# Performance work log

Hardware: AMD Instinct MI355X
Metric: run time of the kernel (lower is better)

Reference implementation:

```python
import jax, jax.numpy as jnp
import numpy as np

N, D, C, O = 65536, 256, 1024, 64

def setup_inputs() -> dict:
    key = jax.random.key(0)
    k1, k2, k3, k4 = jax.random.split(key, 4)
    x = jax.random.normal(k1, (N, D), dtype=jnp.float32)
    centers = jax.random.normal(k2, (C, D), dtype=jnp.float32)
    sigma = jnp.ones((C,), dtype=jnp.float32)
    # nn.Linear(C, O): weight [O, C], bias [O]
    bound = 1.0 / np.sqrt(C)
    W = jax.random.uniform(k3, (O, C), minval=-bound, maxval=bound, dtype=jnp.float32)
    b = jax.random.uniform(k4, (O,), minval=-bound, maxval=bound, dtype=jnp.float32)
    return {"x": x, "centers": centers, "sigma": sigma, "W": W, "b": b}

def reference(x, centers, sigma, W, b):
    # dist_sq[n,c] = ||x_n - c_c||^2, via GEMM identity (same math as sum((x-c)**2))
    x_sq = jnp.sum(x * x, axis=-1, keepdims=True)              # [N,1]
    c_sq = jnp.sum(centers * centers, axis=-1)                 # [C]
    cross = jnp.einsum('nd,cd->nc', x, centers)                # [N,C]
    dist_sq = x_sq - 2.0 * cross + c_sq[None, :]               # [N,C]
    rbf = jnp.exp(-dist_sq / (2.0 * sigma ** 2 + 1e-8))        # [N,C]
    out = jnp.einsum('nc,oc->no', rbf, W) + b                  # [N,O]
    return out
```

## Files before the change

### kernel.cpp

```cpp
#include <hip/hip_runtime.h>
#include <stdint.h>

#define NROWS 65536
#define DIM   256
#define NC    1024
#define NO    64

#define BN    128
#define WROWS 32
#define BC    128
#define NTILE (NC / BC)

using bf16x8 = __bf16 __attribute__((ext_vector_type(8)));
using f32x4  = float __attribute__((ext_vector_type(4)));
using u16x4  = unsigned short __attribute__((ext_vector_type(4)));
using u32x2  = unsigned int __attribute__((ext_vector_type(2)));

#define MFMA16(a, b, c) __builtin_amdgcn_mfma_f32_16x16x32_bf16((a), (b), (c), 0, 0, 0)

__device__ inline unsigned short bf16_bits(float f) {
    __bf16 h = (__bf16)f;
    return __builtin_bit_cast(unsigned short, h);
}

__global__ __launch_bounds__(256) void prep(const float* __restrict__ cent,
                                            const float* __restrict__ sigma,
                                            const float* __restrict__ w,
                                            unsigned short* __restrict__ cbf,
                                            float* __restrict__ a2,
                                            float* __restrict__ acs,
                                            unsigned short* __restrict__ wbf) {
    const int bid = blockIdx.x;
    if (bid < 256) {
        const int wid = threadIdx.x >> 6, lane = threadIdx.x & 63;
        const int c = bid * 4 + wid;
        float4 v = ((const float4*)cent)[(size_t)c * 64 + lane];
        u16x4 o;
        o[0] = bf16_bits(v.x); o[1] = bf16_bits(v.y);
        o[2] = bf16_bits(v.z); o[3] = bf16_bits(v.w);
        const int t = c >> 7, crow = c & 127, kc = lane >> 1;
        *(u16x4*)((char*)cbf + t * 65536 + (kc * 128 + crow) * 16 + (lane & 1) * 8) = o;
        float ss = v.x * v.x + v.y * v.y + v.z * v.z + v.w * v.w;
        #pragma unroll
        for (int off = 32; off; off >>= 1) ss += __shfl_down(ss, off);
        if (lane == 0) {
            float s = sigma[c];
            float al = 1.0f / (2.0f * s * s + 1e-8f);
            a2[c] = 2.0f * al;
            acs[c] = al * ss;
        }
    } else {
        const int o = bid - 256;
        float4 v = ((const float4*)w)[(size_t)o * 256 + threadIdx.x];
        u16x4 u;
        u[0] = bf16_bits(v.x); u[1] = bf16_bits(v.y);
        u[2] = bf16_bits(v.z); u[3] = bf16_bits(v.w);
        *(u16x4*)(wbf + (size_t)o * NC + threadIdx.x * 4) = u;
    }
}

__global__ __launch_bounds__(256, 2) void rbf_main(
    const float* __restrict__ x,
    const __bf16* __restrict__ cbf, const float* __restrict__ a2,
    const float* __restrict__ acs, const __bf16* __restrict__ wbf,
    const float* __restrict__ bias, float* __restrict__ out) {

    __shared__ __bf16 cent_lds[BC * DIM];
    __shared__ __bf16 rbf_lds[4][WROWS * 64];

    const int tid  = threadIdx.x;
    const int wid  = tid >> 6;
    const int lane = tid & 63;
    const int l15  = lane & 15;
    const int hi   = lane >> 4;

    const int rowbase = blockIdx.x * BN + wid * WROWS;

    bf16x8 xf[2][8];
    float hxsq[2];
    #pragma unroll
    for (int nf = 0; nf < 2; ++nf) {
        const float* xr = x + (size_t)(rowbase + nf * 16 + l15) * DIM;
        float ss = 0.f;
        #pragma unroll
        for (int ks = 0; ks < 8; ++ks) {
            float4 a = *(const float4*)(xr + ks * 32 + hi * 8);
            float4 b = *(const float4*)(xr + ks * 32 + hi * 8 + 4);
            bf16x8 f;
            f[0] = (__bf16)a.x; f[1] = (__bf16)a.y; f[2] = (__bf16)a.z; f[3] = (__bf16)a.w;
            f[4] = (__bf16)b.x; f[5] = (__bf16)b.y; f[6] = (__bf16)b.z; f[7] = (__bf16)b.w;
            xf[nf][ks] = f;
            ss += a.x * a.x + a.y * a.y + a.z * a.z + a.w * a.w;
            ss += b.x * b.x + b.y * b.y + b.z * b.z + b.w * b.w;
        }
        ss += __shfl_xor(ss, 16);
        ss += __shfl_xor(ss, 32);
        hxsq[nf] = 0.5f * ss;
    }

    float bo[4];
    #pragma unroll
    for (int of = 0; of < 4; ++of) bo[of] = bias[of * 16 + l15];

    f32x4 oacc[2][4];
    #pragma unroll
    for (int nf = 0; nf < 2; ++nf)
        #pragma unroll
        for (int of = 0; of < 4; ++of) {
            f32x4 z = {0.f, 0.f, 0.f, 0.f};
            oacc[nf][of] = z;
        }

    #pragma unroll 1
    for (int t = 0; t < NTILE; ++t) {
        __syncthreads();
        {
            const char* src = (const char*)cbf + (size_t)t * 65536
                              + (size_t)(wid * 64 + lane) * 16;
            char* dstb = (char*)cent_lds + (wid * 64) * 16;
            #pragma unroll
            for (int i = 0; i < 16; ++i) {
                __builtin_amdgcn_global_load_lds(
                    (const __attribute__((address_space(1))) uint32_t*)(src + i * 4096),
                    (__attribute__((address_space(3))) uint32_t*)(dstb + i * 4096), 16, 0, 0);
            }
        }
        asm volatile("s_waitcnt vmcnt(0)" ::: "memory");
        __syncthreads();

        f32x4 st[8][2];
        #pragma unroll
        for (int c4 = 0; c4 < 8; ++c4)
            #pragma unroll
            for (int nf = 0; nf < 2; ++nf) {
                f32x4 z = {0.f, 0.f, 0.f, 0.f};
                st[c4][nf] = z;
            }
        #pragma unroll
        for (int ks = 0; ks < 8; ++ks) {
            bf16x8 cf[8];
            #pragma unroll
            for (int c4 = 0; c4 < 8; ++c4)
                cf[c4] = *(const bf16x8*)((const char*)cent_lds
                          + ((ks * 4 + hi) * 128 + c4 * 16 + l15) * 16);
            #pragma unroll
            for (int c4 = 0; c4 < 8; ++c4)
                #pragma unroll
                for (int nf = 0; nf < 2; ++nf)
                    st[c4][nf] = MFMA16(cf[c4], xf[nf][ks], st[c4][nf]);
        }

        char* const rbase = (char*)&rbf_lds[wid][0];
        #pragma unroll
        for (int h = 0; h < 2; ++h) {
            #pragma unroll
            for (int c4h = 0; c4h < 4; ++c4h) {
                const int c4 = h * 4 + c4h;
                const int cg = t * BC + c4 * 16 + hi * 4;
                const f32x4 a24 = *(const f32x4*)(a2 + cg);
                const f32x4 ac4 = *(const f32x4*)(acs + cg);
                #pragma unroll
                for (int nf = 0; nf < 2; ++nf) {
                    const f32x4 v = st[c4][nf];
                    float p0 = __expf(a24[0] * (v[0] - hxsq[nf]) - ac4[0]);
                    float p1 = __expf(a24[1] * (v[1] - hxsq[nf]) - ac4[1]);
                    float p2 = __expf(a24[2] * (v[2] - hxsq[nf]) - ac4[2]);
                    float p3 = __expf(a24[3] * (v[3] - hxsq[nf]) - ac4[3]);
                    u32x2 wv;
                    wv[0] = (unsigned)bf16_bits(p0) | ((unsigned)bf16_bits(p1) << 16);
                    wv[1] = (unsigned)bf16_bits(p2) | ((unsigned)bf16_bits(p3) << 16);
                    const int byte = ((c4h * 2 + (hi >> 1)) * 32 + nf * 16 + l15) * 16
                                     + (hi & 1) * 8;
                    *(u32x2*)(rbase + byte) = wv;
                }
            }
            #pragma unroll
            for (int cs = 0; cs < 2; ++cs) {
                bf16x8 pa[2];
                #pragma unroll
                for (int nf = 0; nf < 2; ++nf)
                    pa[nf] = *(const bf16x8*)(rbase
                              + ((cs * 4 + hi) * 32 + nf * 16 + l15) * 16);
                #pragma unroll
                for (int of = 0; of < 4; ++of) {
                    const bf16x8 wb = *(const bf16x8*)(wbf
                        + (size_t)(of * 16 + l15) * NC + t * BC + h * 64 + cs * 32 + hi * 8);
                    #pragma unroll
                    for (int nf = 0; nf < 2; ++nf)
                        oacc[nf][of] = MFMA16(pa[nf], wb, oacc[nf][of]);
                }
            }
        }
    }

    #pragma unroll
    for (int nf = 0; nf < 2; ++nf)
        #pragma unroll
        for (int of = 0; of < 4; ++of)
            #pragma unroll
            for (int r = 0; r < 4; ++r) {
                const int n = rowbase + nf * 16 + hi * 4 + r;
                out[(size_t)n * NO + of * 16 + l15] = oacc[nf][of][r] + bo[of];
            }
}

extern "C" void kernel_launch(void* const* d_in, const int* in_sizes, int n_in,
                              void* d_out, int out_size, void* d_ws, size_t ws_size,
                              hipStream_t stream) {
    const float* x     = (const float*)d_in[0];
    const float* cent  = (const float*)d_in[1];
    const float* sigma = (const float*)d_in[2];
    const float* W     = (const float*)d_in[3];
    const float* b     = (const float*)d_in[4];
    float* out = (float*)d_out;

    char* ws = (char*)d_ws;
    unsigned short* cbf  = (unsigned short*)(ws + 0);
    float*          a2p  = (float*)(ws + 524288);
    float*          acsp = (float*)(ws + 528384);
    unsigned short* wbf  = (unsigned short*)(ws + 532480);

    prep<<<320, 256, 0, stream>>>(cent, sigma, W, cbf, a2p, acsp, wbf);
    rbf_main<<<NROWS / BN, 256, 0, stream>>>(
        x, (const __bf16*)cbf, a2p, acsp, (const __bf16*)wbf, b, out);
}
```

Before: 169.6 us.

## Halve center tile and prefetch next tile during second GEMM

Shrinks the center tile from 128 to 64 rows, which halves the LDS footprint, and restructures the loop. The next tile's global-to-LDS load is now issued after the first GEMM and exp stage, so it overlaps the second (rbf×W) GEMM instead of stalling at the loop top. The first tile is also prefetched before the x fragments are loaded. The first GEMM is reordered per 16-center group, which cuts live accumulator registers. The cost is twice as many barriers and tile iterations.

```diff
diff --git a/kernel.cpp b/kernel.cpp
--- a/kernel.cpp
+++ b/kernel.cpp
@@ -8,7 +8,7 @@
 
 #define BN    128
 #define WROWS 32
-#define BC    128
+#define BC    64
 #define NTILE (NC / BC)
 
 using bf16x8 = __bf16 __attribute__((ext_vector_type(8)));
@@ -38,8 +38,8 @@
         u16x4 o;
         o[0] = bf16_bits(v.x); o[1] = bf16_bits(v.y);
         o[2] = bf16_bits(v.z); o[3] = bf16_bits(v.w);
-        const int t = c >> 7, crow = c & 127, kc = lane >> 1;
-        *(u16x4*)((char*)cbf + t * 65536 + (kc * 128 + crow) * 16 + (lane & 1) * 8) = o;
+        const int t = c >> 6, crow = c & 63, kc = lane >> 1;
+        *(u16x4*)((char*)cbf + t * 32768 + (kc * 64 + crow) * 16 + (lane & 1) * 8) = o;
         float ss = v.x * v.x + v.y * v.y + v.z * v.z + v.w * v.w;
         #pragma unroll
         for (int off = 32; off; off >>= 1) ss += __shfl_down(ss, off);
@@ -66,7 +66,7 @@
     const float* __restrict__ bias, float* __restrict__ out) {
 
     __shared__ __bf16 cent_lds[BC * DIM];
-    __shared__ __bf16 rbf_lds[4][WROWS * 64];
+    __shared__ __bf16 rbf_lds[4][WROWS * BC];
 
     const int tid  = threadIdx.x;
     const int wid  = tid >> 6;
@@ -75,6 +75,20 @@
     const int hi   = lane >> 4;
 
     const int rowbase = blockIdx.x * BN + wid * WROWS;
+
+    auto stage = [&](int t) {
+        const char* src = (const char*)cbf + (size_t)t * 32768
+                          + (size_t)(wid * 64 + lane) * 16;
+        char* dstb = (char*)cent_lds + (wid * 64) * 16;
+        #pragma unroll
+        for (int i = 0; i < 8; ++i) {
+            __builtin_amdgcn_global_load_lds(
+                (const __attribute__((address_space(1))) uint32_t*)(src + i * 4096),
+                (__attribute__((address_space(3))) uint32_t*)(dstb + i * 4096), 16, 0, 0);
+        }
+    };
+
+    stage(0);
 
     bf16x8 xf[2][8];
     float hxsq[2];
@@ -111,86 +125,76 @@
             oacc[nf][of] = z;
         }
 
+    asm volatile("s_waitcnt vmcnt(0)" ::: "memory");
+    __syncthreads();
+
+    char* const rbase = (char*)&rbf_lds[wid][0];
+
     #pragma unroll 1
     for (int t = 0; t < NTILE; ++t) {
+        #pragma unroll
+        for (int c4 = 0; c4 < 4; ++c4) {
+            bf16x8 cf[8];
+            #pragma unroll
+            for (int ks = 0; ks < 8; ++ks)
+                cf[ks] = *(const bf16x8*)((const char*)cent_lds
+                          + ((ks * 4 + hi) * 64 + c4 * 16 + l15) * 16);
+            f32x4 s0 = {0.f, 0.f, 0.f, 0.f};
+            f32x4 s1 = {0.f, 0.f, 0.f, 0.f};
+            #pragma unroll
+            for (int ks = 0; ks < 8; ++ks) {
+                s0 = MFMA16(cf[ks], xf[0][ks], s0);
+                s1 = MFMA16(cf[ks], xf[1][ks], s1);
+            }
+            const int cg = t * BC + c4 * 16 + hi * 4;
+            const f32x4 a24 = *(const f32x4*)(a2 + cg);
+            const f32x4 ac4 = *(const f32x4*)(acs + cg);
+            const int cc0 = (c4 * 2 + (hi >> 1)) * 32;
+            const int sub = (hi & 1) * 8;
+            {
+                float p0 = __expf(a24[0] * (s0[0] - hxsq[0]) - ac4[0]);
+                float p1 = __expf(a24[1] * (s0[1] - hxsq[0]) - ac4[1]);
+                float p2 = __expf(a24[2] * (s0[2] - hxsq[0]) - ac4[2]);
+                float p3 = __expf(a24[3] * (s0[3] - hxsq[0]) - ac4[3]);
+                u32x2 wv;
+                wv[0] = (unsigned)bf16_bits(p0) | ((unsigned)bf16_bits(p1) << 16);
+                wv[1] = (unsigned)bf16_bits(p2) | ((unsigned)bf16_bits(p3) << 16);
+                *(u32x2*)(rbase + (cc0 + l15) * 16 + sub) = wv;
+            }
+            {
+                float p0 = __expf(a24[0] * (s1[0] - hxsq[1]) - ac4[0]);
+                float p1 = __expf(a24[1] * (s1[1] - hxsq[1]) - ac4[1]);
+                float p2 = __expf(a24[2] * (s1[2] - hxsq[1]) - ac4[2]);
+                float p3 = __expf(a24[3] * (s1[3] - hxsq[1]) - ac4[3]);
+                u32x2 wv;
+                wv[0] = (unsigned)bf16_bits(p0) | ((unsigned)bf16_bits(p1) << 16);
+                wv[1] = (unsigned)bf16_bits(p2) | ((unsigned)bf16_bits(p3) << 16);
+                *(u32x2*)(rbase + (cc0 + 16 + l15) * 16 + sub) = wv;
+            }
+        }
+
         __syncthreads();
-        {
-            const char* src = (const char*)cbf + (size_t)t * 65536
-                              + (size_t)(wid * 64 + lane) * 16;
-            char* dstb = (char*)cent_lds + (wid * 64) * 16;
-            #pragma unroll
-            for (int i = 0; i < 16; ++i) {
-                __builtin_amdgcn_global_load_lds(
-                    (const __attribute__((address_space(1))) uint32_t*)(src + i * 4096),
-                    (__attribute__((address_space(3))) uint32_t*)(dstb + i * 4096), 16, 0, 0);
-            }
-        }
+        if (t + 1 < NTILE) stage(t + 1);
+
+        #pragma unroll
+        for (int cs = 0; cs < 2; ++cs) {
+            bf16x8 pa[2];
+            #pragma unroll
+            for (int nf = 0; nf < 2; ++nf)
+                pa[nf] = *(const bf16x8*)(rbase
+                          + ((cs * 4 + hi) * 32 + nf * 16 + l15) * 16);
+            #pragma unroll
+            for (int of = 0; of < 4; ++of) {
+                const bf16x8 wb = *(const bf16x8*)(wbf + (size_t)(of * 16 + l15) * NC
+                                                   + t * BC + cs * 32 + hi * 8);
+                #pragma unroll
+                for (int nf = 0; nf < 2; ++nf)
+                    oacc[nf][of] = MFMA16(pa[nf], wb, oacc[nf][of]);
+            }
+        }
+
         asm volatile("s_waitcnt vmcnt(0)" ::: "memory");
         __syncthreads();
-
-        f32x4 st[8][2];
-        #pragma unroll
-        for (int c4 = 0; c4 < 8; ++c4)
-            #pragma unroll
-            for (int nf = 0; nf < 2; ++nf) {
-                f32x4 z = {0.f, 0.f, 0.f, 0.f};
-                st[c4][nf] = z;
-            }
-        #pragma unroll
-        for (int ks = 0; ks < 8; ++ks) {
-            bf16x8 cf[8];
-            #pragma unroll
-            for (int c4 = 0; c4 < 8; ++c4)
-                cf[c4] = *(const bf16x8*)((const char*)cent_lds
-                          + ((ks * 4 + hi) * 128 + c4 * 16 + l15) * 16);
-            #pragma unroll
-            for (int c4 = 0; c4 < 8; ++c4)
-                #pragma unroll
-                for (int nf = 0; nf < 2; ++nf)
-                    st[c4][nf] = MFMA16(cf[c4], xf[nf][ks], st[c4][nf]);
-        }
-
-        char* const rbase = (char*)&rbf_lds[wid][0];
-        #pragma unroll
-        for (int h = 0; h < 2; ++h) {
-            #pragma unroll
-            for (int c4h = 0; c4h < 4; ++c4h) {
-                const int c4 = h * 4 + c4h;
-                const int cg = t * BC + c4 * 16 + hi * 4;
-                const f32x4 a24 = *(const f32x4*)(a2 + cg);
-                const f32x4 ac4 = *(const f32x4*)(acs + cg);
-                #pragma unroll
-                for (int nf = 0; nf < 2; ++nf) {
-                    const f32x4 v = st[c4][nf];
-                    float p0 = __expf(a24[0] * (v[0] - hxsq[nf]) - ac4[0]);
-                    float p1 = __expf(a24[1] * (v[1] - hxsq[nf]) - ac4[1]);
-                    float p2 = __expf(a24[2] * (v[2] - hxsq[nf]) - ac4[2]);
-                    float p3 = __expf(a24[3] * (v[3] - hxsq[nf]) - ac4[3]);
-                    u32x2 wv;
-                    wv[0] = (unsigned)bf16_bits(p0) | ((unsigned)bf16_bits(p1) << 16);
-                    wv[1] = (unsigned)bf16_bits(p2) | ((unsigned)bf16_bits(p3) << 16);
-                    const int byte = ((c4h * 2 + (hi >> 1)) * 32 + nf * 16 + l15) * 16
-                                     + (hi & 1) * 8;
-                    *(u32x2*)(rbase + byte) = wv;
-                }
-            }
-            #pragma unroll
-            for (int cs = 0; cs < 2; ++cs) {
-                bf16x8 pa[2];
-                #pragma unroll
-                for (int nf = 0; nf < 2; ++nf)
-                    pa[nf] = *(const bf16x8*)(rbase
-                              + ((cs * 4 + hi) * 32 + nf * 16 + l15) * 16);
-                #pragma unroll
-                for (int of = 0; of < 4; ++of) {
-                    const bf16x8 wb = *(const bf16x8*)(wbf
-                        + (size_t)(of * 16 + l15) * NC + t * BC + h * 64 + cs * 32 + hi * 8);
-                    #pragma unroll
-                    for (int nf = 0; nf < 2; ++nf)
-                        oacc[nf][of] = MFMA16(pa[nf], wb, oacc[nf][of]);
-                }
-            }
-        }
     }
 
     #pragma unroll
```

Result: faster. 165.5 us (-2.4%).

## Split work across wave pairs, shrink center tile, overlap next-tile staging

Applied to the files above, without the earlier changes.

The block grows to 512 threads (8 waves) arranged as 4 pairs. Each pair shares 32 rows and the two waves in a pair split the centers and output columns. The center tile shrinks to 64 so that LDS and register use per wave drop, allowing higher occupancy (launch bounds 512,4). The next center tile is loaded into LDS asynchronously while the second GEMM runs, hiding part of the global-load latency. The cost is more block-wide barriers and redundant x loads and norm computation, since both waves of a pair read the same rows.

```diff
diff --git a/kernel.cpp b/kernel.cpp
--- a/kernel.cpp
+++ b/kernel.cpp
@@ -7,8 +7,7 @@
 #define NO    64
 
 #define BN    128
-#define WROWS 32
-#define BC    128
+#define BC    64
 #define NTILE (NC / BC)
 
 using bf16x8 = __bf16 __attribute__((ext_vector_type(8)));
@@ -38,8 +37,8 @@
         u16x4 o;
         o[0] = bf16_bits(v.x); o[1] = bf16_bits(v.y);
         o[2] = bf16_bits(v.z); o[3] = bf16_bits(v.w);
-        const int t = c >> 7, crow = c & 127, kc = lane >> 1;
-        *(u16x4*)((char*)cbf + t * 65536 + (kc * 128 + crow) * 16 + (lane & 1) * 8) = o;
+        const int t = c >> 6, crow = c & 63, kc = lane >> 1;
+        *(u16x4*)((char*)cbf + t * 32768 + (kc * 64 + crow) * 16 + (lane & 1) * 8) = o;
         float ss = v.x * v.x + v.y * v.y + v.z * v.z + v.w * v.w;
         #pragma unroll
         for (int off = 32; off; off >>= 1) ss += __shfl_down(ss, off);
@@ -59,22 +58,37 @@
     }
 }
 
-__global__ __launch_bounds__(256, 2) void rbf_main(
+__global__ __launch_bounds__(512, 4) void rbf_main(
     const float* __restrict__ x,
     const __bf16* __restrict__ cbf, const float* __restrict__ a2,
     const float* __restrict__ acs, const __bf16* __restrict__ wbf,
     const float* __restrict__ bias, float* __restrict__ out) {
 
     __shared__ __bf16 cent_lds[BC * DIM];
-    __shared__ __bf16 rbf_lds[4][WROWS * 64];
+    __shared__ __bf16 rbf_lds[4][32 * BC];
 
     const int tid  = threadIdx.x;
     const int wid  = tid >> 6;
+    const int pair = wid >> 1;
+    const int half = wid & 1;
     const int lane = tid & 63;
     const int l15  = lane & 15;
     const int hi   = lane >> 4;
 
-    const int rowbase = blockIdx.x * BN + wid * WROWS;
+    const int rowbase = blockIdx.x * BN + pair * 32;
+
+    auto stage = [&](int t) {
+        const char* src = (const char*)cbf + (size_t)t * 32768 + (size_t)tid * 16;
+        char* dstb = (char*)cent_lds + (wid * 64) * 16;
+        #pragma unroll
+        for (int i = 0; i < 4; ++i) {
+            __builtin_amdgcn_global_load_lds(
+                (const __attribute__((address_space(1))) uint32_t*)(src + i * 8192),
+                (__attribute__((address_space(3))) uint32_t*)(dstb + i * 8192), 16, 0, 0);
+        }
+    };
+
+    stage(0);
 
     bf16x8 xf[2][8];
     float hxsq[2];
@@ -98,39 +112,29 @@
         hxsq[nf] = 0.5f * ss;
     }
 
-    float bo[4];
-    #pragma unroll
-    for (int of = 0; of < 4; ++of) bo[of] = bias[of * 16 + l15];
-
-    f32x4 oacc[2][4];
+    float bo[2];
+    #pragma unroll
+    for (int of = 0; of < 2; ++of) bo[of] = bias[(half * 2 + of) * 16 + l15];
+
+    f32x4 oacc[2][2];
     #pragma unroll
     for (int nf = 0; nf < 2; ++nf)
         #pragma unroll
-        for (int of = 0; of < 4; ++of) {
+        for (int of = 0; of < 2; ++of) {
             f32x4 z = {0.f, 0.f, 0.f, 0.f};
             oacc[nf][of] = z;
         }
 
+    asm volatile("s_waitcnt vmcnt(0)" ::: "memory");
+    __syncthreads();
+
+    char* const rbase = (char*)&rbf_lds[pair][0];
+
     #pragma unroll 1
     for (int t = 0; t < NTILE; ++t) {
-        __syncthreads();
-        {
-            const char* src = (const char*)cbf + (size_t)t * 65536
-                              + (size_t)(wid * 64 + lane) * 16;
-            char* dstb = (char*)cent_lds + (wid * 64) * 16;
-            #pragma unroll
-            for (int i = 0; i < 16; ++i) {
-                __builtin_amdgcn_global_load_lds(
-                    (const __attribute__((address_space(1))) uint32_t*)(src + i * 4096),
-                    (__attribute__((address_space(3))) uint32_t*)(dstb + i * 4096), 16, 0, 0);
-            }
-        }
-        asm volatile("s_waitcnt vmcnt(0)" ::: "memory");
-        __syncthreads();
-
-        f32x4 st[8][2];
-        #pragma unroll
-        for (int c4 = 0; c4 < 8; ++c4)
+        f32x4 st[2][2];
+        #pragma unroll
+        for (int c4 = 0; c4 < 2; ++c4)
             #pragma unroll
             for (int nf = 0; nf < 2; ++nf) {
                 f32x4 z = {0.f, 0.f, 0.f, 0.f};
@@ -138,69 +142,71 @@
             }
         #pragma unroll
         for (int ks = 0; ks < 8; ++ks) {
-            bf16x8 cf[8];
-            #pragma unroll
-            for (int c4 = 0; c4 < 8; ++c4)
+            bf16x8 cf[2];
+            #pragma unroll
+            for (int c4 = 0; c4 < 2; ++c4)
                 cf[c4] = *(const bf16x8*)((const char*)cent_lds
-                          + ((ks * 4 + hi) * 128 + c4 * 16 + l15) * 16);
-            #pragma unroll
-            for (int c4 = 0; c4 < 8; ++c4)
+                          + ((ks * 4 + hi) * 64 + half * 32 + c4 * 16 + l15) * 16);
+            #pragma unroll
+            for (int c4 = 0; c4 < 2; ++c4)
                 #pragma unroll
                 for (int nf = 0; nf < 2; ++nf)
                     st[c4][nf] = MFMA16(cf[c4], xf[nf][ks], st[c4][nf]);
         }
 
-        char* const rbase = (char*)&rbf_lds[wid][0];
-        #pragma unroll
-        for (int h = 0; h < 2; ++h) {
-            #pragma unroll
-            for (int c4h = 0; c4h < 4; ++c4h) {
-                const int c4 = h * 4 + c4h;
-                const int cg = t * BC + c4 * 16 + hi * 4;
-                const f32x4 a24 = *(const f32x4*)(a2 + cg);
-                const f32x4 ac4 = *(const f32x4*)(acs + cg);
-                #pragma unroll
-                for (int nf = 0; nf < 2; ++nf) {
-                    const f32x4 v = st[c4][nf];
-                    float p0 = __expf(a24[0] * (v[0] - hxsq[nf]) - ac4[0]);
-                    float p1 = __expf(a24[1] * (v[1] - hxsq[nf]) - ac4[1]);
-                    float p2 = __expf(a24[2] * (v[2] - hxsq[nf]) - ac4[2]);
-                    float p3 = __expf(a24[3] * (v[3] - hxsq[nf]) - ac4[3]);
-                    u32x2 wv;
-                    wv[0] = (unsigned)bf16_bits(p0) | ((unsigned)bf16_bits(p1) << 16);
-                    wv[1] = (unsigned)bf16_bits(p2) | ((unsigned)bf16_bits(p3) << 16);
-                    const int byte = ((c4h * 2 + (hi >> 1)) * 32 + nf * 16 + l15) * 16
-                                     + (hi & 1) * 8;
-                    *(u32x2*)(rbase + byte) = wv;
-                }
-            }
-            #pragma unroll
-            for (int cs = 0; cs < 2; ++cs) {
-                bf16x8 pa[2];
+        #pragma unroll
+        for (int c4 = 0; c4 < 2; ++c4) {
+            const int cg = t * BC + half * 32 + c4 * 16 + hi * 4;
+            const f32x4 a24 = *(const f32x4*)(a2 + cg);
+            const f32x4 ac4 = *(const f32x4*)(acs + cg);
+            #pragma unroll
+            for (int nf = 0; nf < 2; ++nf) {
+                const f32x4 v = st[c4][nf];
+                float p0 = __expf(a24[0] * (v[0] - hxsq[nf]) - ac4[0]);
+                float p1 = __expf(a24[1] * (v[1] - hxsq[nf]) - ac4[1]);
+                float p2 = __expf(a24[2] * (v[2] - hxsq[nf]) - ac4[2]);
+                float p3 = __expf(a24[3] * (v[3] - hxsq[nf]) - ac4[3]);
+                u32x2 wv;
+                wv[0] = (unsigned)bf16_bits(p0) | ((unsigned)bf16_bits(p1) << 16);
+                wv[1] = (unsigned)bf16_bits(p2) | ((unsigned)bf16_bits(p3) << 16);
+                const int byte = ((half * 4 + c4 * 2 + (hi >> 1)) * 32 + nf * 16 + l15) * 16
+                                 + (hi & 1) * 8;
+                *(u32x2*)(rbase + byte) = wv;
+            }
+        }
+
+        __syncthreads();
+        if (t + 1 < NTILE) stage(t + 1);
+
+        #pragma unroll
+        for (int cs = 0; cs < 2; ++cs) {
+            bf16x8 pa[2];
+            #pragma unroll
+            for (int nf = 0; nf < 2; ++nf)
+                pa[nf] = *(const bf16x8*)(rbase
+                          + ((cs * 4 + hi) * 32 + nf * 16 + l15) * 16);
+            #pragma unroll
+            for (int of = 0; of < 2; ++of) {
+                const bf16x8 wb = *(const bf16x8*)(wbf
+                    + (size_t)((half * 2 + of) * 16 + l15) * NC + t * BC + cs * 32 + hi * 8);
                 #pragma unroll
                 for (int nf = 0; nf < 2; ++nf)
-                    pa[nf] = *(const bf16x8*)(rbase
-                              + ((cs * 4 + hi) * 32 + nf * 16 + l15) * 16);
-                #pragma unroll
-                for (int of = 0; of < 4; ++of) {
-                    const bf16x8 wb = *(const bf16x8*)(wbf
-                        + (size_t)(of * 16 + l15) * NC + t * BC + h * 64 + cs * 32 + hi * 8);
-                    #pragma unroll
-                    for (int nf = 0; nf < 2; ++nf)
-                        oacc[nf][of] = MFMA16(pa[nf], wb, oacc[nf][of]);
-                }
-            }
-        }
+                    oacc[nf][of] = MFMA16(pa[nf], wb, oacc[nf][of]);
+            }
+        }
+
+        asm volatile("s_waitcnt vmcnt(0)" ::: "memory");
+        __syncthreads();
     }
 
     #pragma unroll
     for (int nf = 0; nf < 2; ++nf)
         #pragma unroll
-        for (int of = 0; of < 4; ++of)
+        for (int of = 0; of < 2; ++of)
             #pragma unroll
             for (int r = 0; r < 4; ++r) {
                 const int n = rowbase + nf * 16 + hi * 4 + r;
-                out[(size_t)n * NO + of * 16 + l15] = oacc[nf][of][r] + bo[of];
+                out[(size_t)n * NO + (half * 2 + of) * 16 + l15] = oacc[nf][of][r] + bo[of];
             }
 }
 
@@ -221,6 +227,6 @@
     unsigned short* wbf  = (unsigned short*)(ws + 532480);
 
     prep<<<320, 256, 0, stream>>>(cent, sigma, W, cbf, a2p, acsp, wbf);
-    rbf_main<<<NROWS / BN, 256, 0, stream>>>(
+    rbf_main<<<NROWS / BN, 512, 0, stream>>>(
         x, (const __bf16*)cbf, a2p, acsp, (const __bf16*)wbf, b, out);
 }
```

Result: no change. 172.3 us (+1.6%).
